# Kernel tuning notes

Hardware: AMD Instinct MI355X
Metric: run time of the kernel (lower is better)

## Reference

```python
import jax, jax.numpy as jnp
import numpy as np

EPS = 1e-5

def _layer_norm(x, gamma, beta):
    mu = jnp.mean(x, axis=-1, keepdims=True)
    var = jnp.mean(jnp.square(x - mu), axis=-1, keepdims=True)
    return (x - mu) * jax.lax.rsqrt(var + EPS) * gamma + beta

def setup_inputs() -> dict:
    key = jax.random.key(0)
    ks = jax.random.split(key, 6)
    B, D, H = 8192, 1024, 1024
    x = jax.random.normal(ks[0], (B, D), dtype=jnp.float32)
    h0 = jax.random.normal(ks[1], (B, H), dtype=jnp.float32)
    c0 = jax.random.normal(ks[2], (B, H), dtype=jnp.float32)
    # learned params (orthogonal init approximated by scaled normal for reference purposes)
    weight_h = jax.random.normal(ks[3], (H, 4 * H), dtype=jnp.float32) / np.sqrt(H)
    weight_x = jax.random.normal(ks[4], (D, 4 * H), dtype=jnp.float32) / np.sqrt(D)
    bias = jnp.zeros((4 * H,), dtype=jnp.float32).at[:H].set(1.0)  # forget-gate bias init to 1
    ln1_g = jnp.ones((4 * H,), jnp.float32); ln1_b = jnp.zeros((4 * H,), jnp.float32)
    ln2_g = jnp.ones((4 * H,), jnp.float32); ln2_b = jnp.zeros((4 * H,), jnp.float32)
    ln3_g = jnp.ones((H,), jnp.float32); ln3_b = jnp.zeros((H,), jnp.float32)
    return {"x": x, "h0": h0, "c0": c0, "weight_h": weight_h, "weight_x": weight_x,
            "bias": bias, "ln1_g": ln1_g, "ln1_b": ln1_b, "ln2_g": ln2_g, "ln2_b": ln2_b,
            "ln3_g": ln3_g, "ln3_b": ln3_b}

def reference(x, h0, c0, weight_h, weight_x, bias, ln1_g, ln1_b, ln2_g, ln2_b, ln3_g, ln3_b):
    # gates: [B, 4H] = LN(h0 @ Wh) + LN(x @ Wx) + bias
    gates = _layer_norm(h0 @ weight_h, ln1_g, ln1_b) + _layer_norm(x @ weight_x, ln2_g, ln2_b) + bias
    H = h0.shape[-1]
    f_g, i_g, o_g, c_g = jnp.split(gates, 4, axis=1)  # forget, in, out, cell
    c1 = jax.nn.sigmoid(f_g) * c0 + jax.nn.sigmoid(i_g) * jnp.tanh(c_g)
    h1 = jax.nn.sigmoid(o_g) * jnp.tanh(_layer_norm(c1, ln3_g, ln3_b))
    return (h1, c1)
```

## Files before the change

kernel.cpp:

```cpp
#include <hip/hip_runtime.h>
#include <cstdint>

#define B_ROWS 8192
#define KDIM 1024
#define N4 4096

typedef __attribute__((ext_vector_type(8))) short short8;
typedef __attribute__((ext_vector_type(4))) float float4v;

__device__ __forceinline__ unsigned short f2bf(float f) {
  union { float f; unsigned int u; } v; v.f = f;
  unsigned int r = v.u + 0x7fffu + ((v.u >> 16) & 1u);
  return (unsigned short)(r >> 16);
}

__device__ __forceinline__ float bf2f(unsigned short s) {
  union { unsigned int u; float f; } v; v.u = ((unsigned int)s) << 16;
  return v.f;
}

__device__ __forceinline__ void async16(const unsigned short* g, unsigned short* l) {
  auto gp = (const __attribute__((address_space(1))) unsigned int*)(uintptr_t)g;
  auto lp = (__attribute__((address_space(3))) unsigned int*)(unsigned int)(uintptr_t)l;
  __builtin_amdgcn_global_load_lds(gp, lp, 16, 0, 0);
}

__device__ __forceinline__ float sigm(float v) { return 1.f / (1.f + expf(-v)); }


__global__ __launch_bounds__(256) void cast_bf16(const float* __restrict__ in0,
                                                 unsigned short* __restrict__ out0,
                                                 const float* __restrict__ in1,
                                                 unsigned short* __restrict__ out1) {
  const float* in = blockIdx.y ? in1 : in0;
  unsigned short* out = blockIdx.y ? out1 : out0;
  int i = (blockIdx.x * 256 + threadIdx.x) * 4;
  float4 v = *(const float4*)(in + i);
  ushort4 o;
  o.x = f2bf(v.x); o.y = f2bf(v.y); o.z = f2bf(v.z); o.w = f2bf(v.w);
  *(ushort4*)(out + i) = o;
}

__global__ __launch_bounds__(256) void transpose_cast(const float* __restrict__ W0,
                                                      unsigned short* __restrict__ Wt0,
                                                      const float* __restrict__ W1,
                                                      unsigned short* __restrict__ Wt1) {
  const float* W = blockIdx.z ? W1 : W0;
  unsigned short* Wt = blockIdx.z ? Wt1 : Wt0;
  __shared__ float tile[32][33];
  int n0 = blockIdx.x * 32;
  int k0 = blockIdx.y * 32;
  int tx = threadIdx.x & 31;
  int ty = threadIdx.x >> 5;
#pragma unroll
  for (int i = 0; i < 32; i += 8)
    tile[ty + i][tx] = W[(size_t)(k0 + ty + i) * N4 + n0 + tx];
  __syncthreads();
#pragma unroll
  for (int i = 0; i < 32; i += 8)
    Wt[(size_t)(n0 + ty + i) * KDIM + k0 + tx] = f2bf(tile[tx][ty + i]);
}


__global__ __launch_bounds__(512, 2) void gemm_bf16(
    const unsigned short* __restrict__ Ah, const unsigned short* __restrict__ Wth,
    unsigned short* __restrict__ Uh,
    const unsigned short* __restrict__ Ax, const unsigned short* __restrict__ Wtx,
    unsigned short* __restrict__ Ux, int row0) {
  const unsigned short* A; const unsigned short* W; unsigned short* U;
  if (blockIdx.z == 0) { A = Ah; W = Wth; U = Uh; } else { A = Ax; W = Wtx; U = Ux; }

  __shared__ unsigned short ldsA[2 * 256 * 64];
  __shared__ unsigned short ldsB[2 * 256 * 64];

  const int tid = threadIdx.x;
  const int wave = tid >> 6;
  const int lane = tid & 63;
  const int wm2 = wave >> 2;
  const int wn4 = wave & 3;

  const int gx = N4 / 256;
  const int nwg = gx * (int)gridDim.y;
  const int f = (int)blockIdx.y * gx + (int)blockIdx.x;
  const int qq = nwg >> 3, rr = nwg & 7;
  const int xcd = f & 7, idx = f >> 3;
  const int wg = (xcd < rr) ? (xcd * (qq + 1) + idx)
                            : (rr * (qq + 1) + (xcd - rr) * qq + idx);
  const int bx = wg & (gx - 1);
  const int by = wg / gx;

  const int m0 = row0 + by * 256;
  const int n0 = bx * 256;

  const int r8 = lane >> 3;
  const int c8 = lane & 7;
  const int g8 = ((c8 - r8) & 7) * 8;
  const int aE = (wave & 3) * 16 + (wave >> 2) * 128;
  const int aL = aE + 64;
  const int bE = (wave >> 1) * 64 + (wave & 1) * 16;
  const int bL = bE + 32;

  const unsigned short* gAe = A + (size_t)(m0 + aE + r8) * KDIM + g8;
  const unsigned short* gAl = A + (size_t)(m0 + aL + r8) * KDIM + g8;
  const unsigned short* gBe = W + (size_t)(n0 + bE + r8) * KDIM + g8;
  const unsigned short* gBl = W + (size_t)(n0 + bL + r8) * KDIM + g8;

  const int lq = lane & 15, lh = lane >> 4;
  const int offA0 = (wm2 * 128 + lq) * 64 + ((lh + lq) & 7) * 8;
  const int offA1 = (wm2 * 128 + lq) * 64 + ((4 + lh + lq) & 7) * 8;
  const int offB0 = (wn4 * 64 + lq) * 64 + ((lh + lq) & 7) * 8;
  const int offB1 = (wn4 * 64 + lq) * 64 + ((4 + lh + lq) & 7) * 8;

  float4v acc[8][4];
  float4v zero = {0.f, 0.f, 0.f, 0.f};
#pragma unroll
  for (int i = 0; i < 8; ++i)
#pragma unroll
    for (int j = 0; j < 4; ++j) acc[i][j] = zero;

#define STAGE2(gptr, lbase, kk)                                   \
  do {                                                            \
    async16((gptr) + (kk), (lbase));                              \
    async16((gptr) + (kk) + 8 * KDIM, (lbase) + 8 * 64);          \
  } while (0)

  STAGE2(gAe, ldsA + aE * 64, 0);
  STAGE2(gBe, ldsB + bE * 64, 0);
  STAGE2(gBl, ldsB + bL * 64, 0);
  STAGE2(gAl, ldsA + aL * 64, 0);
  STAGE2(gAe, ldsA + 16384 + aE * 64, 64);
  STAGE2(gBe, ldsB + 16384 + bE * 64, 64);
  STAGE2(gBl, ldsB + 16384 + bL * 64, 64);
  asm volatile("s_waitcnt vmcnt(10)\n\ts_barrier" ::: "memory");

  short8 aF[4][2], bF[4][2];

#pragma unroll 2
  for (int t = 0; t < KDIM / 64; ++t) {
    const unsigned short* sA = ldsA + (t & 1) * 16384;
    const unsigned short* sB = ldsB + (t & 1) * 16384;
    unsigned short* oA = (unsigned short*)ldsA + ((t + 1) & 1) * 16384;
    unsigned short* cA = (unsigned short*)ldsA + (t & 1) * 16384;
    unsigned short* cB = (unsigned short*)ldsB + (t & 1) * 16384;
    const int kAL = (t + 1) * 64;
    const int kNX = (t + 2) * 64;

#pragma unroll
    for (int mi = 0; mi < 4; ++mi) {
      aF[mi][0] = *(const short8*)(sA + offA0 + mi * 1024);
      aF[mi][1] = *(const short8*)(sA + offA1 + mi * 1024);
    }
#pragma unroll
    for (int ni = 0; ni < 2; ++ni) {
      bF[ni][0] = *(const short8*)(sB + offB0 + ni * 1024);
      bF[ni][1] = *(const short8*)(sB + offB1 + ni * 1024);
    }
    STAGE2(gAl, oA + aL * 64, kAL);
    __builtin_amdgcn_s_setprio(1);
#pragma unroll
    for (int kk = 0; kk < 2; ++kk)
#pragma unroll
      for (int mi = 0; mi < 4; ++mi)
#pragma unroll
        for (int ni = 0; ni < 2; ++ni)
          acc[mi][ni] = __builtin_amdgcn_mfma_f32_16x16x32_bf16(aF[mi][kk], bF[ni][kk], acc[mi][ni], 0, 0, 0);
    __builtin_amdgcn_s_setprio(0);
    asm volatile("s_waitcnt vmcnt(10)\n\ts_barrier" ::: "memory");

#pragma unroll
    for (int ni = 0; ni < 2; ++ni) {
      bF[2 + ni][0] = *(const short8*)(sB + offB0 + (2 + ni) * 1024);
      bF[2 + ni][1] = *(const short8*)(sB + offB1 + (2 + ni) * 1024);
    }
    STAGE2(gAe, cA + aE * 64, kNX);
    __builtin_amdgcn_s_setprio(1);
#pragma unroll
    for (int kk = 0; kk < 2; ++kk)
#pragma unroll
      for (int mi = 0; mi < 4; ++mi)
#pragma unroll
        for (int ni = 0; ni < 2; ++ni)
          acc[mi][2 + ni] = __builtin_amdgcn_mfma_f32_16x16x32_bf16(aF[mi][kk], bF[2 + ni][kk], acc[mi][2 + ni], 0, 0, 0);
    __builtin_amdgcn_s_setprio(0);
    asm volatile("s_waitcnt vmcnt(10)\n\ts_barrier" ::: "memory");

#pragma unroll
    for (int mi = 0; mi < 4; ++mi) {
      aF[mi][0] = *(const short8*)(sA + offA0 + (4 + mi) * 1024);
      aF[mi][1] = *(const short8*)(sA + offA1 + (4 + mi) * 1024);
    }
    STAGE2(gBe, cB + bE * 64, kNX);
    __builtin_amdgcn_s_setprio(1);
#pragma unroll
    for (int kk = 0; kk < 2; ++kk)
#pragma unroll
      for (int mi = 0; mi < 4; ++mi)
#pragma unroll
        for (int ni = 0; ni < 2; ++ni)
          acc[4 + mi][ni] = __builtin_amdgcn_mfma_f32_16x16x32_bf16(aF[mi][kk], bF[ni][kk], acc[4 + mi][ni], 0, 0, 0);
    __builtin_amdgcn_s_setprio(0);
    STAGE2(gBl, cB + bL * 64, kNX);
    __builtin_amdgcn_s_setprio(1);
#pragma unroll
    for (int kk = 0; kk < 2; ++kk)
#pragma unroll
      for (int mi = 0; mi < 4; ++mi)
#pragma unroll
        for (int ni = 0; ni < 2; ++ni)
          acc[4 + mi][2 + ni] = __builtin_amdgcn_mfma_f32_16x16x32_bf16(aF[mi][kk], bF[2 + ni][kk], acc[4 + mi][2 + ni], 0, 0, 0);
    __builtin_amdgcn_s_setprio(0);
    asm volatile("s_waitcnt vmcnt(10)\n\ts_barrier" ::: "memory");
  }
  asm volatile("s_waitcnt vmcnt(0)" ::: "memory");

  const int colc = lane & 15;
  const int rowq = (lane >> 4) * 4;
  unsigned short* Ub = U + (size_t)(by * 256 + wm2 * 128 + rowq) * N4 + n0 + wn4 * 64 + colc;
#pragma unroll
  for (int mi = 0; mi < 8; ++mi)
#pragma unroll
    for (int r = 0; r < 4; ++r) {
      unsigned short* Urow = Ub + (size_t)(mi * 16 + r) * N4;
#pragma unroll
      for (int ni = 0; ni < 4; ++ni) Urow[ni * 16] = f2bf(acc[mi][ni][r]);
    }
}


__global__ __launch_bounds__(256) void fused_ln_lstm(
    const unsigned short* __restrict__ Uh, const unsigned short* __restrict__ Ux,
    const float* __restrict__ c0, const float* __restrict__ bias,
    const float* __restrict__ g1, const float* __restrict__ b1,
    const float* __restrict__ g2, const float* __restrict__ b2,
    const float* __restrict__ g3, const float* __restrict__ b3,
    float* __restrict__ h1o, float* __restrict__ c1o, int row0) {
  const int t = threadIdx.x;
  const int lane = t & 63;
  const int wv = t >> 6;
  const size_t rloc = blockIdx.x;
  const size_t rabs = rloc + (size_t)row0;

  const ushort4* uh = (const ushort4*)(Uh + rloc * N4);
  const ushort4* ux = (const ushort4*)(Ux + rloc * N4);
  float4 cold = ((const float4*)(c0 + rabs * KDIM))[t];

  float4 vh[4], vx[4];
  float sh = 0.f, qh = 0.f, sx = 0.f, qx = 0.f;
#pragma unroll
  for (int k = 0; k < 4; ++k) {
    ushort4 au = uh[k * 256 + t];
    float4 a; a.x = bf2f(au.x); a.y = bf2f(au.y); a.z = bf2f(au.z); a.w = bf2f(au.w);
    vh[k] = a;
    sh += (a.x + a.y) + (a.z + a.w);
    qh += a.x * a.x + a.y * a.y + a.z * a.z + a.w * a.w;
    ushort4 bu = ux[k * 256 + t];
    float4 b; b.x = bf2f(bu.x); b.y = bf2f(bu.y); b.z = bf2f(bu.z); b.w = bf2f(bu.w);
    vx[k] = b;
    sx += (b.x + b.y) + (b.z + b.w);
    qx += b.x * b.x + b.y * b.y + b.z * b.z + b.w * b.w;
  }
  __shared__ float red[4][4];
#pragma unroll
  for (int o = 32; o > 0; o >>= 1) {
    sh += __shfl_down(sh, o); qh += __shfl_down(qh, o);
    sx += __shfl_down(sx, o); qx += __shfl_down(qx, o);
  }
  if (lane == 0) { red[wv][0] = sh; red[wv][1] = qh; red[wv][2] = sx; red[wv][3] = qx; }
  __syncthreads();
  sh = red[0][0] + red[1][0] + red[2][0] + red[3][0];
  qh = red[0][1] + red[1][1] + red[2][1] + red[3][1];
  sx = red[0][2] + red[1][2] + red[2][2] + red[3][2];
  qx = red[0][3] + red[1][3] + red[2][3] + red[3][3];
  const float inv4 = 1.f / 4096.f;
  const float muh = sh * inv4, mux = sx * inv4;
  const float rsh = rsqrtf(qh * inv4 - muh * muh + 1e-5f);
  const float rsx = rsqrtf(qx * inv4 - mux * mux + 1e-5f);

  float4 gate[4];
#pragma unroll
  for (int k = 0; k < 4; ++k) {
    int j = k * 256 + t;
    float4 G1 = ((const float4*)g1)[j], B1 = ((const float4*)b1)[j];
    float4 G2 = ((const float4*)g2)[j], B2 = ((const float4*)b2)[j];
    float4 BB = ((const float4*)bias)[j];
    float4 a = vh[k], b = vx[k], r;
    r.x = (a.x - muh) * rsh * G1.x + B1.x + (b.x - mux) * rsx * G2.x + B2.x + BB.x;
    r.y = (a.y - muh) * rsh * G1.y + B1.y + (b.y - mux) * rsx * G2.y + B2.y + BB.y;
    r.z = (a.z - muh) * rsh * G1.z + B1.z + (b.z - mux) * rsx * G2.z + B2.z + BB.z;
    r.w = (a.w - muh) * rsh * G1.w + B1.w + (b.w - mux) * rsx * G2.w + B2.w + BB.w;
    gate[k] = r;
  }
  float4 fg = gate[0], ig = gate[1], og = gate[2], cg = gate[3];
  float4 c1v;
  c1v.x = sigm(fg.x) * cold.x + sigm(ig.x) * tanhf(cg.x);
  c1v.y = sigm(fg.y) * cold.y + sigm(ig.y) * tanhf(cg.y);
  c1v.z = sigm(fg.z) * cold.z + sigm(ig.z) * tanhf(cg.z);
  c1v.w = sigm(fg.w) * cold.w + sigm(ig.w) * tanhf(cg.w);

  float sc = (c1v.x + c1v.y) + (c1v.z + c1v.w);
  float qc = c1v.x * c1v.x + c1v.y * c1v.y + c1v.z * c1v.z + c1v.w * c1v.w;
#pragma unroll
  for (int o = 32; o > 0; o >>= 1) { sc += __shfl_down(sc, o); qc += __shfl_down(qc, o); }
  __syncthreads();
  if (lane == 0) { red[wv][0] = sc; red[wv][1] = qc; }
  __syncthreads();
  sc = red[0][0] + red[1][0] + red[2][0] + red[3][0];
  qc = red[0][1] + red[1][1] + red[2][1] + red[3][1];
  const float invH = 1.f / 1024.f;
  const float muc = sc * invH;
  const float rsc = rsqrtf(qc * invH - muc * muc + 1e-5f);
  float4 G3 = ((const float4*)g3)[t], B3 = ((const float4*)b3)[t];
  float4 h1v;
  h1v.x = sigm(og.x) * tanhf((c1v.x - muc) * rsc * G3.x + B3.x);
  h1v.y = sigm(og.y) * tanhf((c1v.y - muc) * rsc * G3.y + B3.y);
  h1v.z = sigm(og.z) * tanhf((c1v.z - muc) * rsc * G3.z + B3.z);
  h1v.w = sigm(og.w) * tanhf((c1v.w - muc) * rsc * G3.w + B3.w);

  ((float4*)(h1o + rabs * KDIM))[t] = h1v;
  ((float4*)(c1o + rabs * KDIM))[t] = c1v;
}


extern "C" void kernel_launch(void* const* d_in, const int* in_sizes, int n_in,
                              void* d_out, int out_size, void* d_ws, size_t ws_size,
                              hipStream_t stream) {
  const float* x    = (const float*)d_in[0];
  const float* h0   = (const float*)d_in[1];
  const float* c0   = (const float*)d_in[2];
  const float* Wh   = (const float*)d_in[3];
  const float* Wx   = (const float*)d_in[4];
  const float* bias = (const float*)d_in[5];
  const float* g1   = (const float*)d_in[6];
  const float* b1   = (const float*)d_in[7];
  const float* g2   = (const float*)d_in[8];
  const float* b2   = (const float*)d_in[9];
  const float* g3   = (const float*)d_in[10];
  const float* b3   = (const float*)d_in[11];
  float* h1o = (float*)d_out;
  float* c1o = h1o + (size_t)B_ROWS * KDIM;

  unsigned short* Ah  = (unsigned short*)d_ws;
  unsigned short* Ax  = Ah + (size_t)B_ROWS * KDIM;
  unsigned short* Wth = Ax + (size_t)B_ROWS * KDIM;
  unsigned short* Wtx = Wth + (size_t)N4 * KDIM;
  unsigned short* U = Wtx + (size_t)N4 * KDIM;
  size_t used = ((size_t)B_ROWS * KDIM * 2 + (size_t)N4 * KDIM * 2) * sizeof(unsigned short);
  size_t rem = ws_size > used ? ws_size - used : 0;
  int chunk = (int)(rem / ((size_t)2 * N4 * sizeof(unsigned short)));
  chunk &= ~255;
  if (chunk > B_ROWS) chunk = B_ROWS;
  if (chunk < 256) chunk = 256;

  cast_bf16<<<dim3(B_ROWS * KDIM / 1024, 2), 256, 0, stream>>>(h0, Ah, x, Ax);
  transpose_cast<<<dim3(N4 / 32, KDIM / 32, 2), 256, 0, stream>>>(Wh, Wth, Wx, Wtx);

  for (int r0 = 0; r0 < B_ROWS; r0 += chunk) {
    int rows = chunk;
    if (r0 + rows > B_ROWS) rows = B_ROWS - r0;
    unsigned short* Uh = U;
    unsigned short* Ux = U + (size_t)rows * N4;
    gemm_bf16<<<dim3(N4 / 256, rows / 256, 2), 512, 0, stream>>>(Ah, Wth, Uh, Ax, Wtx, Ux, r0);
    fused_ln_lstm<<<rows, 256, 0, stream>>>(Uh, Ux, c0, bias, g1, b1, g2, b2, g3, b3, h1o, c1o, r0);
  }
}
```

Baseline: 359.5 us.

## Rework GEMM prefetch schedule to one-tile lookahead and use fast sigmoid/tanh

The bf16 GEMM main loop now prefetches only the next K-tile into the other LDS buffer, instead of staging two tiles ahead across both buffers. It adds explicit barriers, lgkmcnt waits and sched_barrier fences around each MFMA group, and waits with vmcnt(4) instead of vmcnt(10). Separately, the LSTM epilogue replaces expf/tanhf with hardware exp2 and rcp intrinsics. The schedule change aims to cut LDS hazards and let compute overlap loads more predictably, but the extra barriers and shorter lookahead may expose more memory latency. The fast math intrinsics trade some precision for cheaper transcendentals.

```diff
diff --git a/kernel.cpp b/kernel.cpp
--- a/kernel.cpp
+++ b/kernel.cpp
@@ -25,7 +25,12 @@
   __builtin_amdgcn_global_load_lds(gp, lp, 16, 0, 0);
 }
 
-__device__ __forceinline__ float sigm(float v) { return 1.f / (1.f + expf(-v)); }
+__device__ __forceinline__ float sigm(float v) {
+  return __builtin_amdgcn_rcpf(1.f + __builtin_amdgcn_exp2f(-1.44269504088896f * v));
+}
+__device__ __forceinline__ float tanh_f(float v) {
+  return 1.f - 2.f * __builtin_amdgcn_rcpf(1.f + __builtin_amdgcn_exp2f(2.88539008177793f * v));
+}
 
 
 __global__ __launch_bounds__(256) void cast_bf16(const float* __restrict__ in0,
@@ -62,6 +67,11 @@
 }
 
 
+#define BAR()    asm volatile("s_barrier" ::: "memory")
+#define LGKM0()  asm volatile("s_waitcnt lgkmcnt(0)" ::: "memory")
+#define VM4BAR() asm volatile("s_waitcnt vmcnt(4)\n\ts_barrier" ::: "memory")
+#define SCHED0() __builtin_amdgcn_sched_barrier(0)
+
 __global__ __launch_bounds__(512, 2) void gemm_bf16(
     const unsigned short* __restrict__ Ah, const unsigned short* __restrict__ Wth,
     unsigned short* __restrict__ Uh,
@@ -128,10 +138,7 @@
   STAGE2(gBe, ldsB + bE * 64, 0);
   STAGE2(gBl, ldsB + bL * 64, 0);
   STAGE2(gAl, ldsA + aL * 64, 0);
-  STAGE2(gAe, ldsA + 16384 + aE * 64, 64);
-  STAGE2(gBe, ldsB + 16384 + bE * 64, 64);
-  STAGE2(gBl, ldsB + 16384 + bL * 64, 64);
-  asm volatile("s_waitcnt vmcnt(10)\n\ts_barrier" ::: "memory");
+  VM4BAR();
 
   short8 aF[4][2], bF[4][2];
 
@@ -139,11 +146,9 @@
   for (int t = 0; t < KDIM / 64; ++t) {
     const unsigned short* sA = ldsA + (t & 1) * 16384;
     const unsigned short* sB = ldsB + (t & 1) * 16384;
-    unsigned short* oA = (unsigned short*)ldsA + ((t + 1) & 1) * 16384;
-    unsigned short* cA = (unsigned short*)ldsA + (t & 1) * 16384;
-    unsigned short* cB = (unsigned short*)ldsB + (t & 1) * 16384;
-    const int kAL = (t + 1) * 64;
-    const int kNX = (t + 2) * 64;
+    unsigned short* nA = (unsigned short*)ldsA + ((t + 1) & 1) * 16384;
+    unsigned short* nB = (unsigned short*)ldsB + ((t + 1) & 1) * 16384;
+    const int kNX = (t + 1) * 64;
 
 #pragma unroll
     for (int mi = 0; mi < 4; ++mi) {
@@ -155,7 +160,8 @@
       bF[ni][0] = *(const short8*)(sB + offB0 + ni * 1024);
       bF[ni][1] = *(const short8*)(sB + offB1 + ni * 1024);
     }
-    STAGE2(gAl, oA + aL * 64, kAL);
+    STAGE2(gAe, nA + aE * 64, kNX);
+    BAR(); LGKM0(); SCHED0();
     __builtin_amdgcn_s_setprio(1);
 #pragma unroll
     for (int kk = 0; kk < 2; ++kk)
@@ -165,14 +171,16 @@
         for (int ni = 0; ni < 2; ++ni)
           acc[mi][ni] = __builtin_amdgcn_mfma_f32_16x16x32_bf16(aF[mi][kk], bF[ni][kk], acc[mi][ni], 0, 0, 0);
     __builtin_amdgcn_s_setprio(0);
-    asm volatile("s_waitcnt vmcnt(10)\n\ts_barrier" ::: "memory");
+    SCHED0();
+    VM4BAR();
 
 #pragma unroll
     for (int ni = 0; ni < 2; ++ni) {
       bF[2 + ni][0] = *(const short8*)(sB + offB0 + (2 + ni) * 1024);
       bF[2 + ni][1] = *(const short8*)(sB + offB1 + (2 + ni) * 1024);
     }
-    STAGE2(gAe, cA + aE * 64, kNX);
+    STAGE2(gBe, nB + bE * 64, kNX);
+    BAR(); LGKM0(); SCHED0();
     __builtin_amdgcn_s_setprio(1);
 #pragma unroll
     for (int kk = 0; kk < 2; ++kk)
@@ -182,14 +190,16 @@
         for (int ni = 0; ni < 2; ++ni)
           acc[mi][2 + ni] = __builtin_amdgcn_mfma_f32_16x16x32_bf16(aF[mi][kk], bF[2 + ni][kk], acc[mi][2 + ni], 0, 0, 0);
     __builtin_amdgcn_s_setprio(0);
-    asm volatile("s_waitcnt vmcnt(10)\n\ts_barrier" ::: "memory");
+    SCHED0();
+    VM4BAR();
 
 #pragma unroll
     for (int mi = 0; mi < 4; ++mi) {
       aF[mi][0] = *(const short8*)(sA + offA0 + (4 + mi) * 1024);
       aF[mi][1] = *(const short8*)(sA + offA1 + (4 + mi) * 1024);
     }
-    STAGE2(gBe, cB + bE * 64, kNX);
+    STAGE2(gBl, nB + bL * 64, kNX);
+    BAR(); LGKM0(); SCHED0();
     __builtin_amdgcn_s_setprio(1);
 #pragma unroll
     for (int kk = 0; kk < 2; ++kk)
@@ -199,7 +209,11 @@
         for (int ni = 0; ni < 2; ++ni)
           acc[4 + mi][ni] = __builtin_amdgcn_mfma_f32_16x16x32_bf16(aF[mi][kk], bF[ni][kk], acc[4 + mi][ni], 0, 0, 0);
     __builtin_amdgcn_s_setprio(0);
-    STAGE2(gBl, cB + bL * 64, kNX);
+    SCHED0();
+    BAR();
+
+    STAGE2(gAl, nA + aL * 64, kNX);
+    BAR(); SCHED0();
     __builtin_amdgcn_s_setprio(1);
 #pragma unroll
     for (int kk = 0; kk < 2; ++kk)
@@ -209,7 +223,8 @@
         for (int ni = 0; ni < 2; ++ni)
           acc[4 + mi][2 + ni] = __builtin_amdgcn_mfma_f32_16x16x32_bf16(aF[mi][kk], bF[2 + ni][kk], acc[4 + mi][2 + ni], 0, 0, 0);
     __builtin_amdgcn_s_setprio(0);
-    asm volatile("s_waitcnt vmcnt(10)\n\ts_barrier" ::: "memory");
+    SCHED0();
+    VM4BAR();
   }
   asm volatile("s_waitcnt vmcnt(0)" ::: "memory");
 
@@ -292,10 +307,10 @@
   }
   float4 fg = gate[0], ig = gate[1], og = gate[2], cg = gate[3];
   float4 c1v;
-  c1v.x = sigm(fg.x) * cold.x + sigm(ig.x) * tanhf(cg.x);
-  c1v.y = sigm(fg.y) * cold.y + sigm(ig.y) * tanhf(cg.y);
-  c1v.z = sigm(fg.z) * cold.z + sigm(ig.z) * tanhf(cg.z);
-  c1v.w = sigm(fg.w) * cold.w + sigm(ig.w) * tanhf(cg.w);
+  c1v.x = sigm(fg.x) * cold.x + sigm(ig.x) * tanh_f(cg.x);
+  c1v.y = sigm(fg.y) * cold.y + sigm(ig.y) * tanh_f(cg.y);
+  c1v.z = sigm(fg.z) * cold.z + sigm(ig.z) * tanh_f(cg.z);
+  c1v.w = sigm(fg.w) * cold.w + sigm(ig.w) * tanh_f(cg.w);
 
   float sc = (c1v.x + c1v.y) + (c1v.z + c1v.w);
   float qc = c1v.x * c1v.x + c1v.y * c1v.y + c1v.z * c1v.z + c1v.w * c1v.w;
@@ -311,10 +326,10 @@
   const float rsc = rsqrtf(qc * invH - muc * muc + 1e-5f);
   float4 G3 = ((const float4*)g3)[t], B3 = ((const float4*)b3)[t];
   float4 h1v;
-  h1v.x = sigm(og.x) * tanhf((c1v.x - muc) * rsc * G3.x + B3.x);
-  h1v.y = sigm(og.y) * tanhf((c1v.y - muc) * rsc * G3.y + B3.y);
-  h1v.z = sigm(og.z) * tanhf((c1v.z - muc) * rsc * G3.z + B3.z);
-  h1v.w = sigm(og.w) * tanhf((c1v.w - muc) * rsc * G3.w + B3.w);
+  h1v.x = sigm(og.x) * tanh_f((c1v.x - muc) * rsc * G3.x + B3.x);
+  h1v.y = sigm(og.y) * tanh_f((c1v.y - muc) * rsc * G3.y + B3.y);
+  h1v.z = sigm(og.z) * tanh_f((c1v.z - muc) * rsc * G3.z + B3.z);
+  h1v.w = sigm(og.w) * tanh_f((c1v.w - muc) * rsc * G3.w + B3.w);
 
   ((float4*)(h1o + rabs * KDIM))[t] = h1v;
   ((float4*)(c1o + rabs * KDIM))[t] = c1v;
```

New measurement: 366.7 us. 2.0% more time.
